# Optimization experiments

Measured on AMD Instinct MI355X. Metric: run time of the kernel, lower is better.

Reference implementation:

```python
import jax, jax.numpy as jnp
import numpy as np

K = 16
NS = [2048, 512, 128]

def _knn(q, r, k):
    # q: [B,M,3] query centers, r: [B,N,3] reference points -> (idx [B,M,k], sqdist [B,M,k])
    d2 = (jnp.sum(q * q, -1)[:, :, None] + jnp.sum(r * r, -1)[:, None, :]
          - 2.0 * jnp.einsum('bmd,bnd->bmn', q, r))
    neg, idx = jax.lax.top_k(-d2, k)
    return idx, jnp.maximum(-neg, 0.0)

def _gather(feat, idx):
    # feat [B,N,C], idx [B,M,k] -> [B,M,k,C]
    return jax.vmap(lambda f, i: f[i])(feat, idx)

def _down(x, pos, n, W1, b1, W2, b2):
    # PointNet++-style TransitionDown: sample n centers, kNN group, rel-pos concat, shared MLP, max-pool
    centers = pos[:, :n]
    idx, _ = _knn(centers, pos, K)
    rel = _gather(pos, idx) - centers[:, :, None, :]           # [B,n,K,3]
    feat = jnp.concatenate([rel, _gather(x, idx)], -1)          # [B,n,K,C+3]
    h = jax.nn.relu(feat @ W1 + b1) @ W2 + b2                   # last_act=False
    return jnp.max(h, axis=2), centers

def _up(xc, pc, prv_feat, prv_pos, W, b):
    # TransitionUp: 3-NN inverse-distance interpolation + skip concat + pointwise conv1d
    idx, d2 = _knn(prv_pos, pc, 3)
    w = 1.0 / (d2 + 1e-8)
    w = w / jnp.sum(w, -1, keepdims=True)
    interp = jnp.sum(_gather(xc, idx) * w[..., None], axis=2)   # [B,Nprv,Cc]
    cat = jnp.concatenate([interp, prv_feat], -1)
    return jax.nn.relu(cat @ W + b)

def setup_inputs() -> dict:
    key = jax.random.key(0)
    ks = jax.random.split(key, 16)
    p = lambda k, s: jax.random.normal(k, s, jnp.float32) * 0.02
    B, N = 4, 8192
    return {
        'x': jax.random.normal(ks[0], (B, N, 3), jnp.float32),
        'pos': jax.random.uniform(ks[1], (B, N, 3), jnp.float32),
        'd0_W1': p(ks[2], (6, 128)),   'd0_b1': jnp.zeros((128,), jnp.float32),
        'd0_W2': p(ks[3], (128, 128)), 'd0_b2': jnp.zeros((128,), jnp.float32),
        'd1_W1': p(ks[4], (131, 256)), 'd1_b1': jnp.zeros((256,), jnp.float32),
        'd1_W2': p(ks[5], (256, 256)), 'd1_b2': jnp.zeros((256,), jnp.float32),
        'd2_W1': p(ks[6], (259, 512)), 'd2_b1': jnp.zeros((512,), jnp.float32),
        'd2_W2': p(ks[7], (512, 512)), 'd2_b2': jnp.zeros((512,), jnp.float32),
        'u0_W': p(ks[8], (768, 256)),  'u0_b': jnp.zeros((256,), jnp.float32),
        'u1_W': p(ks[9], (384, 128)),  'u1_b': jnp.zeros((128,), jnp.float32),
        'u2_W': p(ks[10], (134, 128)), 'u2_b': jnp.zeros((128,), jnp.float32),
        'f_W1': p(ks[11], (128, 128)), 'f_b1': jnp.zeros((128,), jnp.float32),
        'f_W2': p(ks[12], (128, 128)), 'f_b2': jnp.zeros((128,), jnp.float32),
    }

def reference(x, pos, d0_W1, d0_b1, d0_W2, d0_b2, d1_W1, d1_b1, d1_W2, d1_b2,
              d2_W1, d2_b1, d2_W2, d2_b2, u0_W, u0_b, u1_W, u1_b, u2_W, u2_b,
              f_W1, f_b1, f_W2, f_b2):
    pos0, x0 = pos, x
    # encoder (transition-down) with cached (pos, x) per scale
    x1, pos1 = _down(x0, pos0, NS[0], d0_W1, d0_b1, d0_W2, d0_b2)
    x2, pos2 = _down(x1, pos1, NS[1], d1_W1, d1_b1, d1_W2, d1_b2)
    x3, pos3 = _down(x2, pos2, NS[2], d2_W1, d2_b1, d2_W2, d2_b2)
    # decoder (transition-up) consuming the cache in reverse; last level concats raw pos to skip feat
    up = _up(x3, pos3, x2, pos2, u0_W, u0_b)
    up = _up(up, pos2, x1, pos1, u1_W, u1_b)
    prv0 = jnp.concatenate([x0, pos0], -1)
    up = _up(up, pos1, prv0, pos0, u2_W, u2_b)
    # feat_map_layer_out: two pointwise conv1d layers, last_act=False
    out = jax.nn.relu(up @ f_W1 + f_b1) @ f_W2 + f_b2
    return (out, pos0)
```

## Files before the change

### kernel.cpp

```cpp
#include <hip/hip_runtime.h>

#define NFULL 8192
#define BATCH 4

typedef unsigned long long u64;
typedef unsigned int u32;
typedef __attribute__((ext_vector_type(8))) short bf8_t;
typedef __attribute__((ext_vector_type(4))) float f4_t;

__device__ __forceinline__ u32 fbias(float f) {
  u32 u = __float_as_uint(f);
  return (u & 0x80000000u) ? ~u : (u | 0x80000000u);
}
__device__ __forceinline__ float funbias(u32 b) {
  u32 u = (b & 0x80000000u) ? (b & 0x7fffffffu) : ~b;
  return __uint_as_float(u);
}
__device__ __forceinline__ short f2bf(float f) {
  u32 u = __float_as_uint(f);
  u32 r = u + 0x7FFFu + ((u >> 16) & 1u);
  return (short)(r >> 16);
}

__global__ __launch_bounds__(256) void build_grids_kernel(
    const float* __restrict__ pos, float4* __restrict__ sortedA,
    int* __restrict__ csA, float4* __restrict__ sortedB, int* __restrict__ csB) {
  __shared__ int cnt[4096];
  __shared__ int partial[256];
  int which = blockIdx.y, b = blockIdx.x, t = threadIdx.x;
  int NREF = which ? 2048 : 8192;
  int GR = which ? 8 : 16;
  int NC = GR * GR * GR;
  float4* sorted = (which ? sortedB : sortedA) + (size_t)b * NREF;
  int* cs = (which ? csB : csA) + b * (which ? 513 : 4097);
  const float* pb = pos + (size_t)b * NFULL * 3;
  for (int c = t; c < NC; c += 256) cnt[c] = 0;
  __syncthreads();
  for (int p = t; p < NREF; p += 256) {
    float x = pb[p * 3 + 0], y = pb[p * 3 + 1], z = pb[p * 3 + 2];
    int cx = min(max((int)(x * GR), 0), GR - 1);
    int cy = min(max((int)(y * GR), 0), GR - 1);
    int cz = min(max((int)(z * GR), 0), GR - 1);
    atomicAdd(&cnt[(cz * GR + cy) * GR + cx], 1);
  }
  __syncthreads();
  int chunk = (NC + 255) / 256;
  int s = 0;
  for (int i = 0; i < chunk; ++i) {
    int c = t * chunk + i;
    if (c < NC) s += cnt[c];
  }
  partial[t] = s;
  __syncthreads();
  if (t == 0) {
    int run = 0;
    for (int i = 0; i < 256; ++i) { int v = partial[i]; partial[i] = run; run += v; }
  }
  __syncthreads();
  int run = partial[t];
  for (int i = 0; i < chunk; ++i) {
    int c = t * chunk + i;
    if (c < NC) { int v = cnt[c]; cnt[c] = run; run += v; }
  }
  __syncthreads();
  for (int c = t; c < NC; c += 256) cs[c] = cnt[c];
  if (t == 0) cs[NC] = NREF;
  __syncthreads();
  for (int p = t; p < NREF; p += 256) {
    float x = pb[p * 3 + 0], y = pb[p * 3 + 1], z = pb[p * 3 + 2];
    int cx = min(max((int)(x * GR), 0), GR - 1);
    int cy = min(max((int)(y * GR), 0), GR - 1);
    int cz = min(max((int)(z * GR), 0), GR - 1);
    int slot = atomicAdd(&cnt[(cz * GR + cy) * GR + cx], 1);
    sorted[slot] = make_float4(x, y, z, __uint_as_float((u32)p));
  }
}

template<int SL>
__device__ __forceinline__ void group_insert(u32 m16, u64 ck, int slot,
                                             u64& val, u64& tau) {
  if (m16) {
    while (m16) {
      int src = __ffs(m16) - 1;
      m16 &= m16 - 1;
      u64 c = __shfl((unsigned long long)ck, src, 16);
      u64 prev = __shfl_up((unsigned long long)val, 1, SL);
      if (slot == 0) prev = 0ull;
      val = (val <= c) ? val : ((prev <= c) ? c : prev);
    }
    tau = __shfl((unsigned long long)val, SL - 1, SL);
  }
}

template<int SL>
__device__ __forceinline__ void scan_range(const float4* __restrict__ sb,
    int s, int e, float qx, float qy, float qz, float qq,
    int g, int gl, int slot, u64& val, u64& tau) {
  for (int t0 = s; t0 < e; t0 += 16) {
    int j = t0 + gl;
    u64 ck = ~0ull;
    if (j < e) {
      float4 P = sb[j];
      float rr = P.x * P.x + P.y * P.y + P.z * P.z;
      float d2 = qq + rr - 2.0f * (qx * P.x + qy * P.y + qz * P.z);
      ck = ((u64)fbias(d2) << 32) | (u32)__float_as_uint(P.w);
    }
    u64 full = __ballot(ck < tau);
    u32 m16 = (u32)((full >> (g * 16)) & 0xFFFFull);
    group_insert<SL>(m16, ck, slot, val, tau);
  }
}


template<int SL, int KOUT, int GR, int R, int NREF>
__device__ void knn_grid_flat_dev(int vbx,
    const float* __restrict__ pos, const float4* __restrict__ sorted,
    const int* __restrict__ cellStart, int csStride, int Mq,
    int* __restrict__ oidx, float* __restrict__ od2) {
  int b = blockIdx.y;
  int wv = threadIdx.x >> 6, lane = threadIdx.x & 63;
  int g = lane >> 4, gl = lane & 15;
  int q = vbx * 16 + wv * 4 + g;
  const float* pb = pos + (size_t)b * NFULL * 3;
  const float4* sb = sorted + (size_t)b * NREF;
  const int* cs = cellStart + b * csStride;
  float qx = pb[q * 3 + 0], qy = pb[q * 3 + 1], qz = pb[q * 3 + 2];
  float qq = qx * qx + qy * qy + qz * qz;
  int ix = min(max((int)(qx * GR), 0), GR - 1);
  int iy = min(max((int)(qy * GR), 0), GR - 1);
  int iz = min(max((int)(qz * GR), 0), GR - 1);
  int x0 = max(ix - R, 0), x1 = min(ix + R, GR - 1);
  int y0 = max(iy - R, 0), y1 = min(iy + R, GR - 1);
  int z0 = max(iz - R, 0), z1 = min(iz + R, GR - 1);

  int ny = y1 - y0 + 1;
  int nrow = (z1 - z0 + 1) * ny;
  int s_i = 0, len_i = 0;
  if (gl < nrow) {
    int zz = z0 + gl / ny, yy = y0 + gl % ny;
    int c0 = (zz * GR + yy) * GR + x0;
    s_i = cs[c0];
    len_i = cs[c0 + (x1 - x0) + 1] - s_i;
  }
  int p_i = len_i;
#pragma unroll
  for (int st = 1; st < 16; st <<= 1) {
    int o = __shfl_up(p_i, st, 16);
    if (gl >= st) p_i += o;
  }
  int T = __shfl(p_i, 15, 16);
  p_i -= len_i;
  int d_i = s_i - p_i;
  if (gl >= nrow) p_i = 0x7fffffff;

  int slot = gl & (SL - 1);
  u64 val = ~0ull, tau = ~0ull;

  for (int v0 = 0; v0 < T; v0 += 16) {
    int v = v0 + gl;
    int r = 0;
#pragma unroll
    for (int st = 8; st >= 1; st >>= 1) {
      int pc = __shfl(p_i, r + st, 16);
      if (v >= pc) r += st;
    }
    int addr = v + __shfl(d_i, r, 16);
    u64 ck = ~0ull;
    if (v < T) {
      float4 P = sb[addr];
      float rr = P.x * P.x + P.y * P.y + P.z * P.z;
      float d2 = qq + rr - 2.0f * (qx * P.x + qy * P.y + qz * P.z);
      ck = ((u64)fbias(d2) << 32) | (u32)__float_as_uint(P.w);
    }
    u64 full = __ballot(ck < tau);
    u32 m16 = (u32)((full >> (g * 16)) & 0xFFFFull);
    group_insert<SL>(m16, ck, slot, val, tau);
  }

  const float h = 1.0f / GR;
  float m = 1e30f;
  if (x0 > 0)      m = fminf(m, qx - x0 * h);
  if (x1 < GR - 1) m = fminf(m, (x1 + 1) * h - qx);
  if (y0 > 0)      m = fminf(m, qy - y0 * h);
  if (y1 < GR - 1) m = fminf(m, (y1 + 1) * h - qy);
  if (z0 > 0)      m = fminf(m, qz - z0 * h);
  if (z1 < GR - 1) m = fminf(m, (z1 + 1) * h - qz);
  float bound = m * m;
  u64 kv = __shfl((unsigned long long)val, KOUT - 1, SL);
  float kth_d2 = funbias((u32)(kv >> 32));
  if (!(kth_d2 < bound)) {
    int X0 = max(ix - (R + 1), 0), X1 = min(ix + (R + 1), GR - 1);
    int Y0 = max(iy - (R + 1), 0), Y1 = min(iy + (R + 1), GR - 1);
    int Z0 = max(iz - (R + 1), 0), Z1 = min(iz + (R + 1), GR - 1);
    int NY2 = Y1 - Y0 + 1;
    int nrow2 = (Z1 - Z0 + 1) * NY2;
    for (int rr2 = 0; rr2 < nrow2; ++rr2) {
      int zz = Z0 + rr2 / NY2, yy = Y0 + rr2 % NY2;
      int c0 = (zz * GR + yy) * GR;
      bool mid = (zz >= z0 && zz <= z1 && yy >= y0 && yy <= y1);
      int s1 = cs[c0 + X0];
      int e1 = mid ? cs[c0 + x0] : cs[c0 + X1 + 1];
      scan_range<SL>(sb, s1, e1, qx, qy, qz, qq, g, gl, slot, val, tau);
      if (mid) {
        int s2 = cs[c0 + x1 + 1];
        int e2 = cs[c0 + X1 + 1];
        scan_range<SL>(sb, s2, e2, qx, qy, qz, qq, g, gl, slot, val, tau);
      }
    }
    x0 = X0; x1 = X1; y0 = Y0; y1 = Y1; z0 = Z0; z1 = Z1;
    m = 1e30f;
    if (x0 > 0)      m = fminf(m, qx - x0 * h);
    if (x1 < GR - 1) m = fminf(m, (x1 + 1) * h - qx);
    if (y0 > 0)      m = fminf(m, qy - y0 * h);
    if (y1 < GR - 1) m = fminf(m, (y1 + 1) * h - qy);
    if (z0 > 0)      m = fminf(m, qz - z0 * h);
    if (z1 < GR - 1) m = fminf(m, (z1 + 1) * h - qz);
    bound = m * m;
    kv = __shfl((unsigned long long)val, KOUT - 1, SL);
    kth_d2 = funbias((u32)(kv >> 32));
    if (!(kth_d2 < bound)) {
      for (int t0 = 0; t0 < NREF; t0 += 16) {
        int j = t0 + gl;
        u64 ck = ~0ull;
        if (j < NREF) {
          float4 P = sb[j];
          int cx = min(max((int)(P.x * GR), 0), GR - 1);
          int cy = min(max((int)(P.y * GR), 0), GR - 1);
          int cz = min(max((int)(P.z * GR), 0), GR - 1);
          bool inbox = (cx >= x0 && cx <= x1 && cy >= y0 && cy <= y1 &&
                        cz >= z0 && cz <= z1);
          if (!inbox) {
            float rr = P.x * P.x + P.y * P.y + P.z * P.z;
            float d2 = qq + rr - 2.0f * (qx * P.x + qy * P.y + qz * P.z);
            ck = ((u64)fbias(d2) << 32) | (u32)__float_as_uint(P.w);
          }
        }
        u64 full = __ballot(ck < tau);
        u32 m16 = (u32)((full >> (g * 16)) & 0xFFFFull);
        group_insert<SL>(m16, ck, slot, val, tau);
      }
    }
  }

  if (gl < KOUT) {
    size_t base = ((size_t)b * Mq + q) * KOUT;
    oidx[base + gl] = (int)(u32)val;
    od2[base + gl] = fmaxf(funbias((u32)(val >> 32)), 0.0f);
  }
}

template<int SL, int KOUT, int GR, int R, int NREF>
__device__ void knn_grid_rows_dev(int vbx,
    const float* __restrict__ pos, const float4* __restrict__ sorted,
    const int* __restrict__ cellStart, int csStride, int Mq,
    int* __restrict__ oidx, float* __restrict__ od2) {
  int b = blockIdx.y;
  int wv = threadIdx.x >> 6, lane = threadIdx.x & 63;
  int g = lane >> 4, gl = lane & 15;
  int q = vbx * 16 + wv * 4 + g;
  const float* pb = pos + (size_t)b * NFULL * 3;
  const float4* sb = sorted + (size_t)b * NREF;
  const int* cs = cellStart + b * csStride;
  float qx = pb[q * 3 + 0], qy = pb[q * 3 + 1], qz = pb[q * 3 + 2];
  float qq = qx * qx + qy * qy + qz * qz;
  int ix = min(max((int)(qx * GR), 0), GR - 1);
  int iy = min(max((int)(qy * GR), 0), GR - 1);
  int iz = min(max((int)(qz * GR), 0), GR - 1);
  int x0 = max(ix - R, 0), x1 = min(ix + R, GR - 1);
  int y0 = max(iy - R, 0), y1 = min(iy + R, GR - 1);
  int z0 = max(iz - R, 0), z1 = min(iz + R, GR - 1);

  int ny = y1 - y0 + 1;
  int nrow = (z1 - z0 + 1) * ny;
  int sLo = 0, eLo = 0, sHi = 0, eHi = 0;
  if (gl < nrow) {
    int zz = z0 + gl / ny, yy = y0 + gl % ny;
    int c0 = (zz * GR + yy) * GR + x0;
    sLo = cs[c0]; eLo = cs[c0 + (x1 - x0) + 1];
  }
  {
    int i2 = gl + 16;
    if (i2 < nrow) {
      int zz = z0 + i2 / ny, yy = y0 + i2 % ny;
      int c0 = (zz * GR + yy) * GR + x0;
      sHi = cs[c0]; eHi = cs[c0 + (x1 - x0) + 1];
    }
  }

  int slot = gl & (SL - 1);
  u64 val = ~0ull, tau = ~0ull;

  for (int r = 0; r < nrow; ++r) {
    int sa = __shfl(sLo, r & 15, 16);
    int sb2 = __shfl(sHi, r & 15, 16);
    int ea = __shfl(eLo, r & 15, 16);
    int eb = __shfl(eHi, r & 15, 16);
    int s = (r < 16) ? sa : sb2;
    int e = (r < 16) ? ea : eb;
    scan_range<SL>(sb, s, e, qx, qy, qz, qq, g, gl, slot, val, tau);
  }

  const float h = 1.0f / GR;
  float m = 1e30f;
  if (x0 > 0)      m = fminf(m, qx - x0 * h);
  if (x1 < GR - 1) m = fminf(m, (x1 + 1) * h - qx);
  if (y0 > 0)      m = fminf(m, qy - y0 * h);
  if (y1 < GR - 1) m = fminf(m, (y1 + 1) * h - qy);
  if (z0 > 0)      m = fminf(m, qz - z0 * h);
  if (z1 < GR - 1) m = fminf(m, (z1 + 1) * h - qz);
  float bound = m * m;
  u64 kv = __shfl((unsigned long long)val, KOUT - 1, SL);
  float kth_d2 = funbias((u32)(kv >> 32));
  if (!(kth_d2 < bound)) {
    int X0 = max(ix - (R + 1), 0), X1 = min(ix + (R + 1), GR - 1);
    int Y0 = max(iy - (R + 1), 0), Y1 = min(iy + (R + 1), GR - 1);
    int Z0 = max(iz - (R + 1), 0), Z1 = min(iz + (R + 1), GR - 1);
    int NY2 = Y1 - Y0 + 1;
    int nrow2 = (Z1 - Z0 + 1) * NY2;
    for (int rr2 = 0; rr2 < nrow2; ++rr2) {
      int zz = Z0 + rr2 / NY2, yy = Y0 + rr2 % NY2;
      int c0 = (zz * GR + yy) * GR;
      bool mid = (zz >= z0 && zz <= z1 && yy >= y0 && yy <= y1);
      int s1 = cs[c0 + X0];
      int e1 = mid ? cs[c0 + x0] : cs[c0 + X1 + 1];
      scan_range<SL>(sb, s1, e1, qx, qy, qz, qq, g, gl, slot, val, tau);
      if (mid) {
        int s2 = cs[c0 + x1 + 1];
        int e2 = cs[c0 + X1 + 1];
        scan_range<SL>(sb, s2, e2, qx, qy, qz, qq, g, gl, slot, val, tau);
      }
    }
    x0 = X0; x1 = X1; y0 = Y0; y1 = Y1; z0 = Z0; z1 = Z1;
    m = 1e30f;
    if (x0 > 0)      m = fminf(m, qx - x0 * h);
    if (x1 < GR - 1) m = fminf(m, (x1 + 1) * h - qx);
    if (y0 > 0)      m = fminf(m, qy - y0 * h);
    if (y1 < GR - 1) m = fminf(m, (y1 + 1) * h - qy);
    if (z0 > 0)      m = fminf(m, qz - z0 * h);
    if (z1 < GR - 1) m = fminf(m, (z1 + 1) * h - qz);
    bound = m * m;
    kv = __shfl((unsigned long long)val, KOUT - 1, SL);
    kth_d2 = funbias((u32)(kv >> 32));
    if (!(kth_d2 < bound)) {
      for (int t0 = 0; t0 < NREF; t0 += 16) {
        int j = t0 + gl;
        u64 ck = ~0ull;
        if (j < NREF) {
          float4 P = sb[j];
          int cx = min(max((int)(P.x * GR), 0), GR - 1);
          int cy = min(max((int)(P.y * GR), 0), GR - 1);
          int cz = min(max((int)(P.z * GR), 0), GR - 1);
          bool inbox = (cx >= x0 && cx <= x1 && cy >= y0 && cy <= y1 &&
                        cz >= z0 && cz <= z1);
          if (!inbox) {
            float rr = P.x * P.x + P.y * P.y + P.z * P.z;
            float d2 = qq + rr - 2.0f * (qx * P.x + qy * P.y + qz * P.z);
            ck = ((u64)fbias(d2) << 32) | (u32)__float_as_uint(P.w);
          }
        }
        u64 full = __ballot(ck < tau);
        u32 m16 = (u32)((full >> (g * 16)) & 0xFFFFull);
        group_insert<SL>(m16, ck, slot, val, tau);
      }
    }
  }

  if (gl < KOUT) {
    size_t base = ((size_t)b * Mq + q) * KOUT;
    oidx[base + gl] = (int)(u32)val;
    od2[base + gl] = fmaxf(funbias((u32)(val >> 32)), 0.0f);
  }
}

template<int SL, int KOUT>
__device__ void knn_brute_dev(int vbx,
    const float* __restrict__ pos, int Nref, int Mq,
    int* __restrict__ oidx, float* __restrict__ od2) {
  int b = blockIdx.y;
  int wv = threadIdx.x >> 6, lane = threadIdx.x & 63;
  int g = lane >> 4, gl = lane & 15;
  int q = vbx * 16 + wv * 4 + g;
  const float* pb = pos + (size_t)b * NFULL * 3;
  float qx = pb[q * 3 + 0], qy = pb[q * 3 + 1], qz = pb[q * 3 + 2];
  float qq = qx * qx + qy * qy + qz * qz;

  int slot = gl & (SL - 1);
  u64 val = ~0ull, tau = ~0ull;

  for (int t0 = 0; t0 < Nref; t0 += 16) {
    int j = t0 + gl;
    float rx = pb[j * 3 + 0];
    float ry = pb[j * 3 + 1];
    float rz = pb[j * 3 + 2];
    float rr = rx * rx + ry * ry + rz * rz;
    float d2 = qq + rr - 2.0f * (qx * rx + qy * ry + qz * rz);
    u64 ck = ((u64)fbias(d2) << 32) | (u32)j;
    u64 full = __ballot(ck < tau);
    u32 m16 = (u32)((full >> (g * 16)) & 0xFFFFull);
    group_insert<SL>(m16, ck, slot, val, tau);
  }

  if (gl < KOUT) {
    size_t base = ((size_t)b * Mq + q) * KOUT;
    oidx[base + gl] = (int)(u32)val;
    od2[base + gl] = fmaxf(funbias((u32)(val >> 32)), 0.0f);
  }
}

__global__ __launch_bounds__(256) void knn_all_kernel(
    const float* __restrict__ pos,
    const float4* __restrict__ sortedA, const int* __restrict__ csA,
    const float4* __restrict__ sortedB, const int* __restrict__ csB,
    int* __restrict__ idx0,  float* __restrict__ d2s,
    int* __restrict__ idx1,  float* __restrict__ d2s1,
    int* __restrict__ idx2,  float* __restrict__ d2s2,
    int* __restrict__ idxu0, float* __restrict__ d2u0,
    int* __restrict__ idxu1, float* __restrict__ d2u1,
    int* __restrict__ idxu2, float* __restrict__ d2u2) {
  int bx = blockIdx.x;
  if (bx < 128)
    knn_grid_rows_dev<16, 16, 16, 2, 8192>(bx, pos, sortedA, csA, 4097, 2048, idx0, d2s);
  else if (bx < 640)
    knn_grid_flat_dev<4, 3, 8, 1, 2048>(bx - 128, pos, sortedB, csB, 513, 8192, idxu2, d2u2);
  else if (bx < 768)
    knn_brute_dev<4, 3>(bx - 640, pos, 512, 2048, idxu1, d2u1);
  else if (bx < 800)
    knn_grid_rows_dev<16, 16, 8, 2, 2048>(bx - 768, pos, sortedB, csB, 513, 512, idx1, d2s1);
  else if (bx < 832)
    knn_brute_dev<4, 3>(bx - 800, pos, 128, 512, idxu0, d2u0);
  else
    knn_brute_dev<16, 16>(bx - 832, pos, 512, 128, idx2, d2s2);
}

__device__ __forceinline__ void pack_tile_rt(const float* __restrict__ W,
                                             short* __restrict__ outp,
                                             int KDIM, int N, int tile, int lane) {
  int NT = N >> 4;
  int kt = tile / NT, nt = tile - kt * NT;
  int n = nt * 16 + (lane & 15);
  int k0 = kt * 32 + (lane >> 4) * 8;
  bf8_t v;
#pragma unroll
  for (int j = 0; j < 8; ++j) {
    int k = k0 + j;
    v[j] = (k < KDIM) ? f2bf(W[(size_t)k * N + n]) : (short)0;
  }
  *(bf8_t*)(outp + ((size_t)tile * 64 + lane) * 8) = v;
}

__global__ __launch_bounds__(64) void pack_copy_all_kernel(
    const float* d0W1, short* d0W1p, const float* d0W2, short* d0W2p,
    const float* d1W1, short* d1W1p, const float* d1W2, short* d1W2p,
    const float* d2W1, short* d2W1p, const float* d2W2, short* d2W2p,
    const float* u2W, short* u2Wp, const float* fW1, short* fW1p,
    const float* fW2, short* fW2p,
    const float* u0W, short* u0Wp, const float* u1W, short* u1Wp,
    const float* pos, float* posOut) {
  int blk = blockIdx.x, lane = threadIdx.x;
  if      (blk < 8)    pack_tile_rt(d0W1, d0W1p, 6, 128, blk, lane);
  else if (blk < 40)   pack_tile_rt(d0W2, d0W2p, 128, 128, blk - 8, lane);
  else if (blk < 120)  pack_tile_rt(d1W1, d1W1p, 131, 256, blk - 40, lane);
  else if (blk < 248)  pack_tile_rt(d1W2, d1W2p, 256, 256, blk - 120, lane);
  else if (blk < 536)  pack_tile_rt(d2W1, d2W1p, 259, 512, blk - 248, lane);
  else if (blk < 1048) pack_tile_rt(d2W2, d2W2p, 512, 512, blk - 536, lane);
  else if (blk < 1088) pack_tile_rt(u2W, u2Wp, 134, 128, blk - 1048, lane);
  else if (blk < 1120) pack_tile_rt(fW1, fW1p, 128, 128, blk - 1088, lane);
  else if (blk < 1152) pack_tile_rt(fW2, fW2p, 128, 128, blk - 1120, lane);
  else if (blk < 1536) pack_tile_rt(u0W, u0Wp, 768, 256, blk - 1152, lane);
  else if (blk < 1632) pack_tile_rt(u1W, u1Wp, 384, 128, blk - 1536, lane);
  else {
    int base = (blk - 1632) * 256;
#pragma unroll
    for (int j = 0; j < 4; ++j) {
      int i = base + lane + j * 64;
      posOut[i] = pos[i];
    }
  }
}

template<int FEAT, int CIN, int CHID, int FPAD, int QB, int WAVES>
__global__ __launch_bounds__(64 * WAVES) void down_mfma_kernel(
    const float* __restrict__ pos, const float* __restrict__ xin,
    const int* __restrict__ idx,
    const short* __restrict__ W1p, const float* __restrict__ b1,
    const short* __restrict__ W2p, const float* __restrict__ b2,
    float* __restrict__ out, int n, int nprev) {
  const int KT1 = FPAD / 32, NT1 = CHID / 16;
  const int KT2 = CHID / 32, NT2 = CHID / 16;
  __shared__ short sFeat[QB][16][FPAD + 8];
  __shared__ short sH1[QB][16][CHID + 8];
  __shared__ int sIdx[QB][16];
  __shared__ float sCtr[QB][3];
  int b = blockIdx.y, q0 = blockIdx.x * QB;
  int t = threadIdx.x;
  int lane = t & 63, wv = t >> 6;
  const float* pb = pos + (size_t)b * NFULL * 3;
  const float* xb = xin + (size_t)b * nprev * CIN;
  if (t < QB * 16)
    sIdx[t >> 4][t & 15] = idx[((size_t)b * n + q0 + (t >> 4)) * 16 + (t & 15)];
  if (t < QB * 3) sCtr[t / 3][t % 3] = pb[(q0 + t / 3) * 3 + (t % 3)];
  __syncthreads();
  for (int e = t; e < QB * 16 * FPAD; e += 64 * WAVES) {
    int k = e / FPAD, c = e - k * FPAD;
    int qq = k >> 4, kk = k & 15;
    float v = 0.f;
    if (c < 3) v = pb[sIdx[qq][kk] * 3 + c] - sCtr[qq][c];
    else if (c < FEAT) v = xb[(size_t)sIdx[qq][kk] * CIN + (c - 3)];
    sFeat[qq][kk][c] = f2bf(v);
  }
  __syncthreads();

  int col = lane & 15, quad = lane >> 4;
  const bf8_t* W1t = (const bf8_t*)W1p;
  for (int nt = 2 * wv; nt < NT1; nt += 2 * WAVES) {
    f4_t acc[QB][2];
    float bb0 = b1[nt * 16 + col], bb1 = b1[nt * 16 + 16 + col];
#pragma unroll
    for (int q = 0; q < QB; ++q) {
      acc[q][0] = {bb0, bb0, bb0, bb0};
      acc[q][1] = {bb1, bb1, bb1, bb1};
    }
#pragma unroll
    for (int kt = 0; kt < KT1; ++kt) {
      bf8_t bf0 = W1t[(kt * NT1 + nt) * 64 + lane];
      bf8_t bf1 = W1t[(kt * NT1 + nt + 1) * 64 + lane];
#pragma unroll
      for (int q = 0; q < QB; ++q) {
        bf8_t a = *(const bf8_t*)&sFeat[q][col][kt * 32 + quad * 8];
        acc[q][0] = __builtin_amdgcn_mfma_f32_16x16x32_bf16(a, bf0, acc[q][0], 0, 0, 0);
        acc[q][1] = __builtin_amdgcn_mfma_f32_16x16x32_bf16(a, bf1, acc[q][1], 0, 0, 0);
      }
    }
#pragma unroll
    for (int q = 0; q < QB; ++q)
#pragma unroll
      for (int r = 0; r < 4; ++r) {
        sH1[q][quad * 4 + r][nt * 16 + col] = f2bf(fmaxf(acc[q][0][r], 0.f));
        sH1[q][quad * 4 + r][nt * 16 + 16 + col] = f2bf(fmaxf(acc[q][1][r], 0.f));
      }
  }
  __syncthreads();

  const bf8_t* W2t = (const bf8_t*)W2p;
  for (int nt = 2 * wv; nt < NT2; nt += 2 * WAVES) {
    f4_t acc[QB][2];
    float bb0 = b2[nt * 16 + col], bb1 = b2[nt * 16 + 16 + col];
#pragma unroll
    for (int q = 0; q < QB; ++q) {
      acc[q][0] = {bb0, bb0, bb0, bb0};
      acc[q][1] = {bb1, bb1, bb1, bb1};
    }
#pragma unroll
    for (int kt = 0; kt < KT2; ++kt) {
      bf8_t bf0 = W2t[(kt * NT2 + nt) * 64 + lane];
      bf8_t bf1 = W2t[(kt * NT2 + nt + 1) * 64 + lane];
#pragma unroll
      for (int q = 0; q < QB; ++q) {
        bf8_t a = *(const bf8_t*)&sH1[q][col][kt * 32 + quad * 8];
        acc[q][0] = __builtin_amdgcn_mfma_f32_16x16x32_bf16(a, bf0, acc[q][0], 0, 0, 0);
        acc[q][1] = __builtin_amdgcn_mfma_f32_16x16x32_bf16(a, bf1, acc[q][1], 0, 0, 0);
      }
    }
#pragma unroll
    for (int q = 0; q < QB; ++q) {
      float m0 = fmaxf(fmaxf(acc[q][0][0], acc[q][0][1]), fmaxf(acc[q][0][2], acc[q][0][3]));
      float m1 = fmaxf(fmaxf(acc[q][1][0], acc[q][1][1]), fmaxf(acc[q][1][2], acc[q][1][3]));
      m0 = fmaxf(m0, __shfl_xor(m0, 16, 64));
      m0 = fmaxf(m0, __shfl_xor(m0, 32, 64));
      m1 = fmaxf(m1, __shfl_xor(m1, 16, 64));
      m1 = fmaxf(m1, __shfl_xor(m1, 32, 64));
      if (lane < 16) {
        float* ob = out + ((size_t)b * n + q0 + q) * CHID;
        ob[nt * 16 + lane] = m0;
        ob[nt * 16 + 16 + lane] = m1;
      }
    }
  }
}

template<int CIN, int CPRV, int COUT, int WPB>
__global__ __launch_bounds__(64 * WPB) void up_mfma_kernel(
    const float* __restrict__ xc, int ncoarse,
    const int* __restrict__ idx3, const float* __restrict__ d23,
    const float* __restrict__ prv, const short* __restrict__ Wp,
    const float* __restrict__ bvec, float* __restrict__ out, int m) {
  const int CTOT = CIN + CPRV;
  const int KT = CTOT / 32, NT = COUT / 16;
  __shared__ short sA[16][CTOT + 8];
  __shared__ float sWt[16][3];
  __shared__ int   sIt[16][3];
  int b = blockIdx.y, q0 = blockIdx.x * 16, t = threadIdx.x;
  int lane = t & 63, wv = t >> 6;
  if (t < 16) {
    size_t base = ((size_t)b * m + q0 + t) * 3;
    float d0 = d23[base + 0], d1 = d23[base + 1], d2v = d23[base + 2];
    float w0 = 1.f / (d0 + 1e-8f), w1 = 1.f / (d1 + 1e-8f), w2 = 1.f / (d2v + 1e-8f);
    float s = w0 + w1 + w2;
    sWt[t][0] = w0 / s; sWt[t][1] = w1 / s; sWt[t][2] = w2 / s;
    sIt[t][0] = idx3[base + 0]; sIt[t][1] = idx3[base + 1]; sIt[t][2] = idx3[base + 2];
  }
  __syncthreads();
  const float* xb = xc + (size_t)b * ncoarse * CIN;
  const float* pvb = prv + ((size_t)b * m + q0) * CPRV;
  for (int e = t; e < 16 * CIN; e += 64 * WPB) {
    int p = e / CIN, c = e % CIN;
    float v = sWt[p][0] * xb[(size_t)sIt[p][0] * CIN + c]
            + sWt[p][1] * xb[(size_t)sIt[p][1] * CIN + c]
            + sWt[p][2] * xb[(size_t)sIt[p][2] * CIN + c];
    sA[p][c] = f2bf(v);
  }
  for (int e = t; e < 16 * CPRV; e += 64 * WPB) {
    int p = e / CPRV, c = e % CPRV;
    sA[p][CIN + c] = f2bf(pvb[(size_t)p * CPRV + c]);
  }
  __syncthreads();
  int col = lane & 15, quad = lane >> 4;
  const bf8_t* Wt = (const bf8_t*)Wp;
  float* ob = out + ((size_t)b * m + q0) * COUT;
  for (int nt = 2 * wv; nt < NT; nt += 2 * WPB) {
    float bb0 = bvec[nt * 16 + col], bb1 = bvec[nt * 16 + 16 + col];
    f4_t acc0 = {bb0, bb0, bb0, bb0}, acc1 = {bb1, bb1, bb1, bb1};
#pragma unroll
    for (int kt = 0; kt < KT; ++kt) {
      bf8_t a = *(const bf8_t*)&sA[col][kt * 32 + quad * 8];
      bf8_t bf0 = Wt[(kt * NT + nt) * 64 + lane];
      bf8_t bf1 = Wt[(kt * NT + nt + 1) * 64 + lane];
      acc0 = __builtin_amdgcn_mfma_f32_16x16x32_bf16(a, bf0, acc0, 0, 0, 0);
      acc1 = __builtin_amdgcn_mfma_f32_16x16x32_bf16(a, bf1, acc1, 0, 0, 0);
    }
#pragma unroll
    for (int r = 0; r < 4; ++r) {
      ob[(size_t)(quad * 4 + r) * COUT + nt * 16 + col] = fmaxf(acc0[r], 0.f);
      ob[(size_t)(quad * 4 + r) * COUT + nt * 16 + 16 + col] = fmaxf(acc1[r], 0.f);
    }
  }
}

__global__ __launch_bounds__(128) void up2f_mfma_kernel(
    const float* __restrict__ xc,
    const int* __restrict__ idx3, const float* __restrict__ d23,
    const float* __restrict__ x0, const float* __restrict__ pos0,
    const short* __restrict__ u2Wp, const float* __restrict__ u2b,
    const short* __restrict__ fW1p, const float* __restrict__ fb1,
    const short* __restrict__ fW2p, const float* __restrict__ fb2,
    float* __restrict__ out) {
  __shared__ short sA[16][168];
  __shared__ short sB[16][136];
  __shared__ float sWt[16][3];
  __shared__ int   sIt[16][3];
  int b = blockIdx.y, q0 = blockIdx.x * 16, t = threadIdx.x;
  int lane = t & 63, wv = t >> 6;
  if (t < 16) {
    size_t base = ((size_t)b * NFULL + q0 + t) * 3;
    float d0 = d23[base + 0], d1 = d23[base + 1], d2v = d23[base + 2];
    float w0 = 1.f / (d0 + 1e-8f), w1 = 1.f / (d1 + 1e-8f), w2 = 1.f / (d2v + 1e-8f);
    float s = w0 + w1 + w2;
    sWt[t][0] = w0 / s; sWt[t][1] = w1 / s; sWt[t][2] = w2 / s;
    sIt[t][0] = idx3[base + 0]; sIt[t][1] = idx3[base + 1]; sIt[t][2] = idx3[base + 2];
  }
  __syncthreads();
  const float* xb = xc + (size_t)b * 2048 * 128;
#pragma unroll
  for (int p = 0; p < 16; ++p) {
    float v = sWt[p][0] * xb[(size_t)sIt[p][0] * 128 + t]
            + sWt[p][1] * xb[(size_t)sIt[p][1] * 128 + t]
            + sWt[p][2] * xb[(size_t)sIt[p][2] * 128 + t];
    sA[p][t] = f2bf(v);
  }
  for (int e = t; e < 16 * 32; e += 128) {
    int p = e / 32, c = 128 + (e % 32);
    float v = 0.f;
    if (c < 131) v = x0[((size_t)b * NFULL + q0 + p) * 3 + (c - 128)];
    else if (c < 134) v = pos0[((size_t)b * NFULL + q0 + p) * 3 + (c - 131)];
    sA[p][c] = f2bf(v);
  }
  __syncthreads();
  int col = lane & 15, quad = lane >> 4;

  bf8_t a1[5];
#pragma unroll
  for (int kt = 0; kt < 5; ++kt)
    a1[kt] = *(const bf8_t*)&sA[col][kt * 32 + quad * 8];
  const bf8_t* W1t = (const bf8_t*)u2Wp;
  for (int nt = 2 * wv; nt < 8; nt += 4) {
    float bb0 = u2b[nt * 16 + col], bb1 = u2b[nt * 16 + 16 + col];
    f4_t acc0 = {bb0, bb0, bb0, bb0}, acc1 = {bb1, bb1, bb1, bb1};
#pragma unroll
    for (int kt = 0; kt < 5; ++kt) {
      bf8_t bf0 = W1t[(kt * 8 + nt) * 64 + lane];
      bf8_t bf1 = W1t[(kt * 8 + nt + 1) * 64 + lane];
      acc0 = __builtin_amdgcn_mfma_f32_16x16x32_bf16(a1[kt], bf0, acc0, 0, 0, 0);
      acc1 = __builtin_amdgcn_mfma_f32_16x16x32_bf16(a1[kt], bf1, acc1, 0, 0, 0);
    }
#pragma unroll
    for (int r = 0; r < 4; ++r) {
      sB[quad * 4 + r][nt * 16 + col] = f2bf(fmaxf(acc0[r], 0.f));
      sB[quad * 4 + r][nt * 16 + 16 + col] = f2bf(fmaxf(acc1[r], 0.f));
    }
  }
  __syncthreads();

  bf8_t a2[4];
#pragma unroll
  for (int kt = 0; kt < 4; ++kt)
    a2[kt] = *(const bf8_t*)&sB[col][kt * 32 + quad * 8];
  const bf8_t* W2t = (const bf8_t*)fW1p;
  for (int nt = 2 * wv; nt < 8; nt += 4) {
    float bb0 = fb1[nt * 16 + col], bb1 = fb1[nt * 16 + 16 + col];
    f4_t acc0 = {bb0, bb0, bb0, bb0}, acc1 = {bb1, bb1, bb1, bb1};
#pragma unroll
    for (int kt = 0; kt < 4; ++kt) {
      bf8_t bf0 = W2t[(kt * 8 + nt) * 64 + lane];
      bf8_t bf1 = W2t[(kt * 8 + nt + 1) * 64 + lane];
      acc0 = __builtin_amdgcn_mfma_f32_16x16x32_bf16(a2[kt], bf0, acc0, 0, 0, 0);
      acc1 = __builtin_amdgcn_mfma_f32_16x16x32_bf16(a2[kt], bf1, acc1, 0, 0, 0);
    }
#pragma unroll
    for (int r = 0; r < 4; ++r) {
      sA[quad * 4 + r][nt * 16 + col] = f2bf(fmaxf(acc0[r], 0.f));
      sA[quad * 4 + r][nt * 16 + 16 + col] = f2bf(fmaxf(acc1[r], 0.f));
    }
  }
  __syncthreads();

  bf8_t a3[4];
#pragma unroll
  for (int kt = 0; kt < 4; ++kt)
    a3[kt] = *(const bf8_t*)&sA[col][kt * 32 + quad * 8];
  const bf8_t* W3t = (const bf8_t*)fW2p;
  float* ob = out + ((size_t)b * NFULL + q0) * 128;
  for (int nt = 2 * wv; nt < 8; nt += 4) {
    float bb0 = fb2[nt * 16 + col], bb1 = fb2[nt * 16 + 16 + col];
    f4_t acc0 = {bb0, bb0, bb0, bb0}, acc1 = {bb1, bb1, bb1, bb1};
#pragma unroll
    for (int kt = 0; kt < 4; ++kt) {
      bf8_t bf0 = W3t[(kt * 8 + nt) * 64 + lane];
      bf8_t bf1 = W3t[(kt * 8 + nt + 1) * 64 + lane];
      acc0 = __builtin_amdgcn_mfma_f32_16x16x32_bf16(a3[kt], bf0, acc0, 0, 0, 0);
      acc1 = __builtin_amdgcn_mfma_f32_16x16x32_bf16(a3[kt], bf1, acc1, 0, 0, 0);
    }
#pragma unroll
    for (int r = 0; r < 4; ++r) {
      ob[(size_t)(quad * 4 + r) * 128 + nt * 16 + col] = acc0[r];
      ob[(size_t)(quad * 4 + r) * 128 + nt * 16 + 16 + col] = acc1[r];
    }
  }
}

extern "C" void kernel_launch(void* const* d_in, const int* in_sizes, int n_in,
                              void* d_out, int out_size, void* d_ws, size_t ws_size,
                              hipStream_t stream) {
  const float* x    = (const float*)d_in[0];
  const float* pos  = (const float*)d_in[1];
  const float* d0W1 = (const float*)d_in[2];
  const float* d0b1 = (const float*)d_in[3];
  const float* d0W2 = (const float*)d_in[4];
  const float* d0b2 = (const float*)d_in[5];
  const float* d1W1 = (const float*)d_in[6];
  const float* d1b1 = (const float*)d_in[7];
  const float* d1W2 = (const float*)d_in[8];
  const float* d1b2 = (const float*)d_in[9];
  const float* d2W1 = (const float*)d_in[10];
  const float* d2b1 = (const float*)d_in[11];
  const float* d2W2 = (const float*)d_in[12];
  const float* d2b2 = (const float*)d_in[13];
  const float* u0W  = (const float*)d_in[14];
  const float* u0b  = (const float*)d_in[15];
  const float* u1W  = (const float*)d_in[16];
  const float* u1b  = (const float*)d_in[17];
  const float* u2W  = (const float*)d_in[18];
  const float* u2b  = (const float*)d_in[19];
  const float* fW1  = (const float*)d_in[20];
  const float* fb1  = (const float*)d_in[21];
  const float* fW2  = (const float*)d_in[22];
  const float* fb2  = (const float*)d_in[23];

  char* ws = (char*)d_ws;
  float* x1    = (float*)(ws + 0);
  float* x2    = (float*)(ws + 4194304);
  float* x3    = (float*)(ws + 6291456);
  float* up0o  = (float*)(ws + 7340032);
  float* up1o  = (float*)(ws + 9437184);
  int*   idx0  = (int*)  (ws + 13631488);
  int*   idx1  = (int*)  (ws + 14155776);
  int*   idx2  = (int*)  (ws + 14286848);
  float* d2s   = (float*)(ws + 14319616);
  int*   idxu0 = (int*)  (ws + 14843904);
  float* d2u0  = (float*)(ws + 14868480);
  int*   idxu1 = (int*)  (ws + 14893056);
  float* d2u1  = (float*)(ws + 14991360);
  int*   idxu2 = (int*)  (ws + 15089664);
  float* d2u2  = (float*)(ws + 15482880);
  short* d1W1p = (short*)(ws + 15876096);
  short* d1W2p = (short*)(ws + 15958016);
  short* d2W1p = (short*)(ws + 16089088);
  short* d2W2p = (short*)(ws + 16384000);
  short* d0W1p = (short*)(ws + 16908288);
  short* d0W2p = (short*)(ws + 16916480);
  float4* sortedA = (float4*)(ws + 16949248);
  int*    csA     = (int*)   (ws + 17473536);
  float4* sortedB = (float4*)(ws + 17539136);
  int*    csB     = (int*)   (ws + 17670208);
  short* u2Wp  = (short*)(ws + 17697920);
  short* fW1p  = (short*)(ws + 17738880);
  short* fW2p  = (short*)(ws + 17771648);
  float* d2s1  = (float*)(ws + 17804416);
  float* d2s2  = (float*)(ws + 17935488);

  float* out = (float*)d_out;
  short* u0Wp = (short*)out;
  short* u1Wp = (short*)(out + 98304);

  pack_copy_all_kernel<<<dim3(2016), 64, 0, stream>>>(
      d0W1, d0W1p, d0W2, d0W2p, d1W1, d1W1p, d1W2, d1W2p,
      d2W1, d2W1p, d2W2, d2W2p, u2W, u2Wp, fW1, fW1p, fW2, fW2p,
      u0W, u0Wp, u1W, u1Wp,
      pos, out + (size_t)BATCH * NFULL * 128);
  build_grids_kernel<<<dim3(BATCH, 2), 256, 0, stream>>>(pos, sortedA, csA, sortedB, csB);

  knn_all_kernel<<<dim3(840, BATCH), 256, 0, stream>>>(
      pos, sortedA, csA, sortedB, csB,
      idx0, d2s, idx1, d2s1, idx2, d2s2,
      idxu0, d2u0, idxu1, d2u1, idxu2, d2u2);

  down_mfma_kernel<6, 3, 128, 32, 4, 4><<<dim3(512, BATCH), 256, 0, stream>>>(
      pos, x, idx0, d0W1p, d0b1, d0W2p, d0b2, x1, 2048, 8192);
  down_mfma_kernel<131, 128, 256, 160, 4, 8><<<dim3(128, BATCH), 512, 0, stream>>>(
      pos, x1, idx1, d1W1p, d1b1, d1W2p, d1b2, x2, 512, 2048);
  down_mfma_kernel<259, 256, 512, 288, 2, 8><<<dim3(64, BATCH), 512, 0, stream>>>(
      pos, x2, idx2, d2W1p, d2b1, d2W2p, d2b2, x3, 128, 512);

  up_mfma_kernel<512, 256, 256, 4><<<dim3(32, BATCH), 256, 0, stream>>>(
      x3, 128, idxu0, d2u0, x2, u0Wp, u0b, up0o, 512);
  up_mfma_kernel<256, 128, 128, 2><<<dim3(128, BATCH), 128, 0, stream>>>(
      up0o, 512, idxu1, d2u1, x1, u1Wp, u1b, up1o, 2048);
  up2f_mfma_kernel<<<dim3(512, BATCH), 128, 0, stream>>>(
      up1o, idxu2, d2u2, x, pos, u2Wp, u2b, fW1p, fb1, fW2p, fb2, out);
}
```

Before: 322.7 us.

## Add 512-point grid, flatten 32-row kNN scans, reorder kNN block dispatch

Builds a third spatial grid over the 512-point level so the up1 3-NN search, previously brute force over 512 points, becomes a grid search. The row-by-row kNN scan for K=16 queries is replaced with a flattened 32-row prefix-sum traversal, so each 16-lane group works on full chunks instead of per-row partial chunks. Unused distance outputs for the down-path kNNs are skipped, and the block dispatch order in the fused kNN kernel puts the heavy K=16 searches first. The cost is extra shuffles in the binary search and one more grid-building block row.

```diff
diff --git a/kernel.cpp b/kernel.cpp
--- a/kernel.cpp
+++ b/kernel.cpp
@@ -24,15 +24,18 @@
 
 __global__ __launch_bounds__(256) void build_grids_kernel(
     const float* __restrict__ pos, float4* __restrict__ sortedA,
-    int* __restrict__ csA, float4* __restrict__ sortedB, int* __restrict__ csB) {
+    int* __restrict__ csA, float4* __restrict__ sortedB, int* __restrict__ csB,
+    float4* __restrict__ sortedC, int* __restrict__ csC) {
   __shared__ int cnt[4096];
   __shared__ int partial[256];
   int which = blockIdx.y, b = blockIdx.x, t = threadIdx.x;
-  int NREF = which ? 2048 : 8192;
-  int GR = which ? 8 : 16;
+  int NREF = (which == 0) ? 8192 : (which == 1) ? 2048 : 512;
+  int GR = (which == 0) ? 16 : 8;
   int NC = GR * GR * GR;
-  float4* sorted = (which ? sortedB : sortedA) + (size_t)b * NREF;
-  int* cs = (which ? csB : csA) + b * (which ? 513 : 4097);
+  float4* sorted = ((which == 0) ? sortedA : (which == 1) ? sortedB : sortedC)
+                   + (size_t)b * NREF;
+  int* cs = ((which == 0) ? csA + b * 4097 : (which == 1) ? csB + b * 513
+                                           : csC + b * 513);
   const float* pb = pos + (size_t)b * NFULL * 3;
   for (int c = t; c < NC; c += 256) cnt[c] = 0;
   __syncthreads();
@@ -113,70 +116,11 @@
 
 
 template<int SL, int KOUT, int GR, int R, int NREF>
-__device__ void knn_grid_flat_dev(int vbx,
-    const float* __restrict__ pos, const float4* __restrict__ sorted,
-    const int* __restrict__ cellStart, int csStride, int Mq,
-    int* __restrict__ oidx, float* __restrict__ od2) {
-  int b = blockIdx.y;
-  int wv = threadIdx.x >> 6, lane = threadIdx.x & 63;
-  int g = lane >> 4, gl = lane & 15;
-  int q = vbx * 16 + wv * 4 + g;
-  const float* pb = pos + (size_t)b * NFULL * 3;
-  const float4* sb = sorted + (size_t)b * NREF;
-  const int* cs = cellStart + b * csStride;
-  float qx = pb[q * 3 + 0], qy = pb[q * 3 + 1], qz = pb[q * 3 + 2];
-  float qq = qx * qx + qy * qy + qz * qz;
-  int ix = min(max((int)(qx * GR), 0), GR - 1);
-  int iy = min(max((int)(qy * GR), 0), GR - 1);
-  int iz = min(max((int)(qz * GR), 0), GR - 1);
-  int x0 = max(ix - R, 0), x1 = min(ix + R, GR - 1);
-  int y0 = max(iy - R, 0), y1 = min(iy + R, GR - 1);
-  int z0 = max(iz - R, 0), z1 = min(iz + R, GR - 1);
-
-  int ny = y1 - y0 + 1;
-  int nrow = (z1 - z0 + 1) * ny;
-  int s_i = 0, len_i = 0;
-  if (gl < nrow) {
-    int zz = z0 + gl / ny, yy = y0 + gl % ny;
-    int c0 = (zz * GR + yy) * GR + x0;
-    s_i = cs[c0];
-    len_i = cs[c0 + (x1 - x0) + 1] - s_i;
-  }
-  int p_i = len_i;
-#pragma unroll
-  for (int st = 1; st < 16; st <<= 1) {
-    int o = __shfl_up(p_i, st, 16);
-    if (gl >= st) p_i += o;
-  }
-  int T = __shfl(p_i, 15, 16);
-  p_i -= len_i;
-  int d_i = s_i - p_i;
-  if (gl >= nrow) p_i = 0x7fffffff;
-
-  int slot = gl & (SL - 1);
-  u64 val = ~0ull, tau = ~0ull;
-
-  for (int v0 = 0; v0 < T; v0 += 16) {
-    int v = v0 + gl;
-    int r = 0;
-#pragma unroll
-    for (int st = 8; st >= 1; st >>= 1) {
-      int pc = __shfl(p_i, r + st, 16);
-      if (v >= pc) r += st;
-    }
-    int addr = v + __shfl(d_i, r, 16);
-    u64 ck = ~0ull;
-    if (v < T) {
-      float4 P = sb[addr];
-      float rr = P.x * P.x + P.y * P.y + P.z * P.z;
-      float d2 = qq + rr - 2.0f * (qx * P.x + qy * P.y + qz * P.z);
-      ck = ((u64)fbias(d2) << 32) | (u32)__float_as_uint(P.w);
-    }
-    u64 full = __ballot(ck < tau);
-    u32 m16 = (u32)((full >> (g * 16)) & 0xFFFFull);
-    group_insert<SL>(m16, ck, slot, val, tau);
-  }
-
+__device__ __forceinline__ void knn_tail(
+    const float4* __restrict__ sb, const int* __restrict__ cs,
+    float qx, float qy, float qz, float qq,
+    int ix, int iy, int iz, int x0, int x1, int y0, int y1, int z0, int z1,
+    int g, int gl, int slot, u64& val, u64& tau) {
   const float h = 1.0f / GR;
   float m = 1e30f;
   if (x0 > 0)      m = fminf(m, qx - x0 * h);
@@ -241,16 +185,10 @@
       }
     }
   }
-
-  if (gl < KOUT) {
-    size_t base = ((size_t)b * Mq + q) * KOUT;
-    oidx[base + gl] = (int)(u32)val;
-    od2[base + gl] = fmaxf(funbias((u32)(val >> 32)), 0.0f);
-  }
 }
 
 template<int SL, int KOUT, int GR, int R, int NREF>
-__device__ void knn_grid_rows_dev(int vbx,
+__device__ void knn_grid_flat_dev(int vbx,
     const float* __restrict__ pos, const float4* __restrict__ sorted,
     const int* __restrict__ cellStart, int csStride, int Mq,
     int* __restrict__ oidx, float* __restrict__ od2) {
@@ -272,103 +210,147 @@
 
   int ny = y1 - y0 + 1;
   int nrow = (z1 - z0 + 1) * ny;
-  int sLo = 0, eLo = 0, sHi = 0, eHi = 0;
+  int s_i = 0, len_i = 0;
   if (gl < nrow) {
     int zz = z0 + gl / ny, yy = y0 + gl % ny;
     int c0 = (zz * GR + yy) * GR + x0;
-    sLo = cs[c0]; eLo = cs[c0 + (x1 - x0) + 1];
+    s_i = cs[c0];
+    len_i = cs[c0 + (x1 - x0) + 1] - s_i;
+  }
+  int p_i = len_i;
+#pragma unroll
+  for (int st = 1; st < 16; st <<= 1) {
+    int o = __shfl_up(p_i, st, 16);
+    if (gl >= st) p_i += o;
+  }
+  int T = __shfl(p_i, 15, 16);
+  p_i -= len_i;
+  int d_i = s_i - p_i;
+  if (gl >= nrow) p_i = 0x7fffffff;
+
+  int slot = gl & (SL - 1);
+  u64 val = ~0ull, tau = ~0ull;
+
+  for (int v0 = 0; v0 < T; v0 += 16) {
+    int v = v0 + gl;
+    int r = 0;
+#pragma unroll
+    for (int st = 8; st >= 1; st >>= 1) {
+      int pc = __shfl(p_i, r + st, 16);
+      if (v >= pc) r += st;
+    }
+    int addr = v + __shfl(d_i, r, 16);
+    u64 ck = ~0ull;
+    if (v < T) {
+      float4 P = sb[addr];
+      float rr = P.x * P.x + P.y * P.y + P.z * P.z;
+      float d2 = qq + rr - 2.0f * (qx * P.x + qy * P.y + qz * P.z);
+      ck = ((u64)fbias(d2) << 32) | (u32)__float_as_uint(P.w);
+    }
+    u64 full = __ballot(ck < tau);
+    u32 m16 = (u32)((full >> (g * 16)) & 0xFFFFull);
+    group_insert<SL>(m16, ck, slot, val, tau);
+  }
+
+  knn_tail<SL, KOUT, GR, R, NREF>(sb, cs, qx, qy, qz, qq,
+      ix, iy, iz, x0, x1, y0, y1, z0, z1, g, gl, slot, val, tau);
+
+  if (gl < KOUT) {
+    size_t base = ((size_t)b * Mq + q) * KOUT;
+    oidx[base + gl] = (int)(u32)val;
+    if (od2) od2[base + gl] = fmaxf(funbias((u32)(val >> 32)), 0.0f);
+  }
+}
+
+template<int SL, int KOUT, int GR, int R, int NREF>
+__device__ void knn_grid_flat32_dev(int vbx,
+    const float* __restrict__ pos, const float4* __restrict__ sorted,
+    const int* __restrict__ cellStart, int csStride, int Mq,
+    int* __restrict__ oidx, float* __restrict__ od2) {
+  int b = blockIdx.y;
+  int wv = threadIdx.x >> 6, lane = threadIdx.x & 63;
+  int g = lane >> 4, gl = lane & 15;
+  int q = vbx * 16 + wv * 4 + g;
+  const float* pb = pos + (size_t)b * NFULL * 3;
+  const float4* sb = sorted + (size_t)b * NREF;
+  const int* cs = cellStart + b * csStride;
+  float qx = pb[q * 3 + 0], qy = pb[q * 3 + 1], qz = pb[q * 3 + 2];
+  float qq = qx * qx + qy * qy + qz * qz;
+  int ix = min(max((int)(qx * GR), 0), GR - 1);
+  int iy = min(max((int)(qy * GR), 0), GR - 1);
+  int iz = min(max((int)(qz * GR), 0), GR - 1);
+  int x0 = max(ix - R, 0), x1 = min(ix + R, GR - 1);
+  int y0 = max(iy - R, 0), y1 = min(iy + R, GR - 1);
+  int z0 = max(iz - R, 0), z1 = min(iz + R, GR - 1);
+
+  int ny = y1 - y0 + 1;
+  int nrow = (z1 - z0 + 1) * ny;
+  int sLo = 0, lenLo = 0, sHi = 0, lenHi = 0;
+  if (gl < nrow) {
+    int zz = z0 + gl / ny, yy = y0 + gl % ny;
+    int c0 = (zz * GR + yy) * GR + x0;
+    sLo = cs[c0]; lenLo = cs[c0 + (x1 - x0) + 1] - sLo;
   }
   {
     int i2 = gl + 16;
     if (i2 < nrow) {
       int zz = z0 + i2 / ny, yy = y0 + i2 % ny;
       int c0 = (zz * GR + yy) * GR + x0;
-      sHi = cs[c0]; eHi = cs[c0 + (x1 - x0) + 1];
-    }
-  }
+      sHi = cs[c0]; lenHi = cs[c0 + (x1 - x0) + 1] - sHi;
+    }
+  }
+  int pLo = lenLo, pHi = lenHi;
+#pragma unroll
+  for (int st = 1; st < 16; st <<= 1) {
+    int o = __shfl_up(pLo, st, 16);
+    if (gl >= st) pLo += o;
+    int o2 = __shfl_up(pHi, st, 16);
+    if (gl >= st) pHi += o2;
+  }
+  int tot16 = __shfl(pLo, 15, 16);
+  pHi += tot16;
+  int T = __shfl(pHi, 15, 16);
+  pLo -= lenLo; pHi -= lenHi;
+  int dLo = sLo - pLo, dHi = sHi - pHi;
+  if (gl >= nrow) pLo = 0x7fffffff;
+  if (gl + 16 >= nrow) pHi = 0x7fffffff;
 
   int slot = gl & (SL - 1);
   u64 val = ~0ull, tau = ~0ull;
 
-  for (int r = 0; r < nrow; ++r) {
-    int sa = __shfl(sLo, r & 15, 16);
-    int sb2 = __shfl(sHi, r & 15, 16);
-    int ea = __shfl(eLo, r & 15, 16);
-    int eb = __shfl(eHi, r & 15, 16);
-    int s = (r < 16) ? sa : sb2;
-    int e = (r < 16) ? ea : eb;
-    scan_range<SL>(sb, s, e, qx, qy, qz, qq, g, gl, slot, val, tau);
-  }
-
-  const float h = 1.0f / GR;
-  float m = 1e30f;
-  if (x0 > 0)      m = fminf(m, qx - x0 * h);
-  if (x1 < GR - 1) m = fminf(m, (x1 + 1) * h - qx);
-  if (y0 > 0)      m = fminf(m, qy - y0 * h);
-  if (y1 < GR - 1) m = fminf(m, (y1 + 1) * h - qy);
-  if (z0 > 0)      m = fminf(m, qz - z0 * h);
-  if (z1 < GR - 1) m = fminf(m, (z1 + 1) * h - qz);
-  float bound = m * m;
-  u64 kv = __shfl((unsigned long long)val, KOUT - 1, SL);
-  float kth_d2 = funbias((u32)(kv >> 32));
-  if (!(kth_d2 < bound)) {
-    int X0 = max(ix - (R + 1), 0), X1 = min(ix + (R + 1), GR - 1);
-    int Y0 = max(iy - (R + 1), 0), Y1 = min(iy + (R + 1), GR - 1);
-    int Z0 = max(iz - (R + 1), 0), Z1 = min(iz + (R + 1), GR - 1);
-    int NY2 = Y1 - Y0 + 1;
-    int nrow2 = (Z1 - Z0 + 1) * NY2;
-    for (int rr2 = 0; rr2 < nrow2; ++rr2) {
-      int zz = Z0 + rr2 / NY2, yy = Y0 + rr2 % NY2;
-      int c0 = (zz * GR + yy) * GR;
-      bool mid = (zz >= z0 && zz <= z1 && yy >= y0 && yy <= y1);
-      int s1 = cs[c0 + X0];
-      int e1 = mid ? cs[c0 + x0] : cs[c0 + X1 + 1];
-      scan_range<SL>(sb, s1, e1, qx, qy, qz, qq, g, gl, slot, val, tau);
-      if (mid) {
-        int s2 = cs[c0 + x1 + 1];
-        int e2 = cs[c0 + X1 + 1];
-        scan_range<SL>(sb, s2, e2, qx, qy, qz, qq, g, gl, slot, val, tau);
-      }
-    }
-    x0 = X0; x1 = X1; y0 = Y0; y1 = Y1; z0 = Z0; z1 = Z1;
-    m = 1e30f;
-    if (x0 > 0)      m = fminf(m, qx - x0 * h);
-    if (x1 < GR - 1) m = fminf(m, (x1 + 1) * h - qx);
-    if (y0 > 0)      m = fminf(m, qy - y0 * h);
-    if (y1 < GR - 1) m = fminf(m, (y1 + 1) * h - qy);
-    if (z0 > 0)      m = fminf(m, qz - z0 * h);
-    if (z1 < GR - 1) m = fminf(m, (z1 + 1) * h - qz);
-    bound = m * m;
-    kv = __shfl((unsigned long long)val, KOUT - 1, SL);
-    kth_d2 = funbias((u32)(kv >> 32));
-    if (!(kth_d2 < bound)) {
-      for (int t0 = 0; t0 < NREF; t0 += 16) {
-        int j = t0 + gl;
-        u64 ck = ~0ull;
-        if (j < NREF) {
-          float4 P = sb[j];
-          int cx = min(max((int)(P.x * GR), 0), GR - 1);
-          int cy = min(max((int)(P.y * GR), 0), GR - 1);
-          int cz = min(max((int)(P.z * GR), 0), GR - 1);
-          bool inbox = (cx >= x0 && cx <= x1 && cy >= y0 && cy <= y1 &&
-                        cz >= z0 && cz <= z1);
-          if (!inbox) {
-            float rr = P.x * P.x + P.y * P.y + P.z * P.z;
-            float d2 = qq + rr - 2.0f * (qx * P.x + qy * P.y + qz * P.z);
-            ck = ((u64)fbias(d2) << 32) | (u32)__float_as_uint(P.w);
-          }
-        }
-        u64 full = __ballot(ck < tau);
-        u32 m16 = (u32)((full >> (g * 16)) & 0xFFFFull);
-        group_insert<SL>(m16, ck, slot, val, tau);
-      }
-    }
-  }
+  for (int v0 = 0; v0 < T; v0 += 16) {
+    int v = v0 + gl;
+    int r = 0;
+#pragma unroll
+    for (int st = 16; st >= 1; st >>= 1) {
+      int j = r + st;
+      int pcL = __shfl(pLo, j & 15, 16);
+      int pcH = __shfl(pHi, j & 15, 16);
+      int pc = (j < 16) ? pcL : pcH;
+      if (v >= pc) r = j;
+    }
+    int dL = __shfl(dLo, r & 15, 16);
+    int dH = __shfl(dHi, r & 15, 16);
+    int addr = v + ((r < 16) ? dL : dH);
+    u64 ck = ~0ull;
+    if (v < T) {
+      float4 P = sb[addr];
+      float rr = P.x * P.x + P.y * P.y + P.z * P.z;
+      float d2 = qq + rr - 2.0f * (qx * P.x + qy * P.y + qz * P.z);
+      ck = ((u64)fbias(d2) << 32) | (u32)__float_as_uint(P.w);
+    }
+    u64 full = __ballot(ck < tau);
+    u32 m16 = (u32)((full >> (g * 16)) & 0xFFFFull);
+    group_insert<SL>(m16, ck, slot, val, tau);
+  }
+
+  knn_tail<SL, KOUT, GR, R, NREF>(sb, cs, qx, qy, qz, qq,
+      ix, iy, iz, x0, x1, y0, y1, z0, z1, g, gl, slot, val, tau);
 
   if (gl < KOUT) {
     size_t base = ((size_t)b * Mq + q) * KOUT;
     oidx[base + gl] = (int)(u32)val;
-    od2[base + gl] = fmaxf(funbias((u32)(val >> 32)), 0.0f);
+    if (od2) od2[base + gl] = fmaxf(funbias((u32)(val >> 32)), 0.0f);
   }
 }
 
@@ -403,7 +385,7 @@
   if (gl < KOUT) {
     size_t base = ((size_t)b * Mq + q) * KOUT;
     oidx[base + gl] = (int)(u32)val;
-    od2[base + gl] = fmaxf(funbias((u32)(val >> 32)), 0.0f);
+    if (od2) od2[base + gl] = fmaxf(funbias((u32)(val >> 32)), 0.0f);
   }
 }
 
@@ -411,25 +393,24 @@
     const float* __restrict__ pos,
     const float4* __restrict__ sortedA, const int* __restrict__ csA,
     const float4* __restrict__ sortedB, const int* __restrict__ csB,
-    int* __restrict__ idx0,  float* __restrict__ d2s,
-    int* __restrict__ idx1,  float* __restrict__ d2s1,
-    int* __restrict__ idx2,  float* __restrict__ d2s2,
+    const float4* __restrict__ sortedC, const int* __restrict__ csC,
+    int* __restrict__ idx0, int* __restrict__ idx1, int* __restrict__ idx2,
     int* __restrict__ idxu0, float* __restrict__ d2u0,
     int* __restrict__ idxu1, float* __restrict__ d2u1,
     int* __restrict__ idxu2, float* __restrict__ d2u2) {
   int bx = blockIdx.x;
-  if (bx < 128)
-    knn_grid_rows_dev<16, 16, 16, 2, 8192>(bx, pos, sortedA, csA, 4097, 2048, idx0, d2s);
-  else if (bx < 640)
-    knn_grid_flat_dev<4, 3, 8, 1, 2048>(bx - 128, pos, sortedB, csB, 513, 8192, idxu2, d2u2);
-  else if (bx < 768)
-    knn_brute_dev<4, 3>(bx - 640, pos, 512, 2048, idxu1, d2u1);
-  else if (bx < 800)
-    knn_grid_rows_dev<16, 16, 8, 2, 2048>(bx - 768, pos, sortedB, csB, 513, 512, idx1, d2s1);
-  else if (bx < 832)
-    knn_brute_dev<4, 3>(bx - 800, pos, 128, 512, idxu0, d2u0);
+  if (bx < 8)
+    knn_brute_dev<16, 16>(bx, pos, 512, 128, idx2, nullptr);
+  else if (bx < 40)
+    knn_grid_flat32_dev<16, 16, 8, 2, 2048>(bx - 8, pos, sortedB, csB, 513, 512, idx1, nullptr);
+  else if (bx < 168)
+    knn_grid_flat32_dev<16, 16, 16, 2, 8192>(bx - 40, pos, sortedA, csA, 4097, 2048, idx0, nullptr);
+  else if (bx < 296)
+    knn_grid_flat32_dev<4, 3, 8, 2, 512>(bx - 168, pos, sortedC, csC, 513, 2048, idxu1, d2u1);
+  else if (bx < 808)
+    knn_grid_flat_dev<4, 3, 8, 1, 2048>(bx - 296, pos, sortedB, csB, 513, 8192, idxu2, d2u2);
   else
-    knn_brute_dev<16, 16>(bx - 832, pos, 512, 128, idx2, d2s2);
+    knn_brute_dev<4, 3>(bx - 808, pos, 128, 512, idxu0, d2u0);
 }
 
 __device__ __forceinline__ void pack_tile_rt(const float* __restrict__ W,
@@ -784,7 +765,8 @@
   int*   idx0  = (int*)  (ws + 13631488);
   int*   idx1  = (int*)  (ws + 14155776);
   int*   idx2  = (int*)  (ws + 14286848);
-  float* d2s   = (float*)(ws + 14319616);
+  float4* sortedC = (float4*)(ws + 14319616);
+  int*    csC     = (int*)   (ws + 14352384);
   int*   idxu0 = (int*)  (ws + 14843904);
   float* d2u0  = (float*)(ws + 14868480);
   int*   idxu1 = (int*)  (ws + 14893056);
@@ -804,8 +786,6 @@
   short* u2Wp  = (short*)(ws + 17697920);
   short* fW1p  = (short*)(ws + 17738880);
   short* fW2p  = (short*)(ws + 17771648);
-  float* d2s1  = (float*)(ws + 17804416);
-  float* d2s2  = (float*)(ws + 17935488);
 
   float* out = (float*)d_out;
   short* u0Wp = (short*)out;
@@ -816,11 +796,12 @@
       d2W1, d2W1p, d2W2, d2W2p, u2W, u2Wp, fW1, fW1p, fW2, fW2p,
       u0W, u0Wp, u1W, u1Wp,
       pos, out + (size_t)BATCH * NFULL * 128);
-  build_grids_kernel<<<dim3(BATCH, 2), 256, 0, stream>>>(pos, sortedA, csA, sortedB, csB);
+  build_grids_kernel<<<dim3(BATCH, 3), 256, 0, stream>>>(
+      pos, sortedA, csA, sortedB, csB, sortedC, csC);
 
   knn_all_kernel<<<dim3(840, BATCH), 256, 0, stream>>>(
-      pos, sortedA, csA, sortedB, csB,
-      idx0, d2s, idx1, d2s1, idx2, d2s2,
+      pos, sortedA, csA, sortedB, csB, sortedC, csC,
+      idx0, idx1, idx2,
       idxu0, d2u0, idxu1, d2u1, idxu2, d2u2);
 
   down_mfma_kernel<6, 3, 128, 32, 4, 4><<<dim3(512, BATCH), 256, 0, stream>>>(
```

Measured after the change: 312.3 us. 1.03x faster.
